# Performance work log

Measured on AMD Instinct MI355X. Metric: run time of the kernel, lower is better.

The kernel has to match this reference:

```python
import jax, jax.numpy as jnp
import numpy as np
from jax import lax

MARGIN = 0.2
NMAX = 1


def setup_inputs() -> dict:
    key = jax.random.key(0)
    k1, k2 = jax.random.split(key)
    N, D = 8192, 512
    imgs = jax.random.normal(k1, (N, D), dtype=jnp.float32)
    caps = jax.random.normal(k2, (N, D), dtype=jnp.float32)
    return {"imgs": imgs, "caps": caps}


def reference(imgs, caps):
    # scores[i, j] = <img_i, cap_j>  -> [N, N]
    scores = jnp.matmul(imgs, caps.T)
    diag = jnp.diagonal(scores)  # [N]
    s = scores - 2.0 * jnp.diag(diag)
    # top-nmax over columns (axis 0): hardest negative captions per caption slot
    max_c = lax.top_k(s.T, NMAX)[0].T  # [NMAX, N]
    # top-nmax over rows (axis 1): hardest negative images per image slot
    max_i = lax.top_k(s, NMAX)[0]      # [N, NMAX]
    neg_cap = jnp.sum(jnp.maximum(max_c + (MARGIN - diag)[None, :], 0.0))
    neg_img = jnp.sum(jnp.maximum(max_i + (MARGIN - diag)[:, None], 0.0))
    return neg_cap + neg_img
```

## Files before the change

### kernel.cpp

```cpp
#include <hip/hip_runtime.h>

#define N_ROWS 8192
#define DIM    512

typedef __attribute__((ext_vector_type(4))) float frag_cd;
typedef __attribute__((ext_vector_type(4))) int   v4i;
typedef __attribute__((ext_vector_type(8))) int   v8i;

__device__ __forceinline__ unsigned f2fp8(float x) {
    float a = fabsf(x);
    unsigned s = (__float_as_uint(x) >> 31) << 7;
    if (a < 0.015625f) return s;
    a = fminf(a, 448.f);
    unsigned u = __float_as_uint(a);
    u += 0x7FFFFu + ((u >> 20) & 1u);
    unsigned exp = (u >> 23) - 120u;
    unsigned mant = (u >> 20) & 7u;
    return s | (exp << 3) | mant;
}
__device__ __forceinline__ unsigned pack4fp8(float4 v) {
    return f2fp8(v.x) | (f2fp8(v.y) << 8) | (f2fp8(v.z) << 16) | (f2fp8(v.w) << 24);
}
__device__ __forceinline__ unsigned enc_f32(float f) {
    unsigned u = __float_as_uint(f);
    return (u & 0x80000000u) ? ~u : (u | 0x80000000u);
}
__device__ __forceinline__ float dec_f32(unsigned k) {
    return __uint_as_float((k & 0x80000000u) ? (k & 0x7FFFFFFFu) : ~k);
}


__global__ __launch_bounds__(256) void k_prep(const float* __restrict__ imgs,
                                              const float* __restrict__ caps,
                                              unsigned char* __restrict__ fimgs,
                                              unsigned char* __restrict__ fcaps,
                                              float* __restrict__ diag,
                                              unsigned* __restrict__ rowmax,
                                              unsigned* __restrict__ colmax,
                                              float* __restrict__ out) {
    const int b  = blockIdx.x;
    const int cr = b >> 2;
    const int t  = threadIdx.x;
    const int w = t >> 6, l = t & 63;
    const int row = ((b & 3) << 2) + w;
    if (b == 0 && t == 0) out[0] = 0.f;
    const int r = cr * 16 + row;
    const float* ar = imgs + (size_t)r * DIM + l * 8;
    const float* br = caps + (size_t)r * DIM + l * 8;
    float4 a0 = *(const float4*)ar, a1 = *(const float4*)(ar + 4);
    float4 b0 = *(const float4*)br, b1 = *(const float4*)(br + 4);
    uint2 oa, ob;
    oa.x = pack4fp8(a0); oa.y = pack4fp8(a1);
    ob.x = pack4fp8(b0); ob.y = pack4fp8(b1);
    const size_t addr = (size_t)cr * 8192 + (size_t)((l >> 4) << 11)
                      + (((l >> 1) & 1) << 10)
                      + ((((l >> 2) & 3) << 4) + row) * 16 + ((l & 1) << 3);
    *(uint2*)(fimgs + addr) = oa;
    *(uint2*)(fcaps + addr) = ob;
    float s = a0.x * b0.x + a0.y * b0.y + a0.z * b0.z + a0.w * b0.w
            + a1.x * b1.x + a1.y * b1.y + a1.z * b1.z + a1.w * b1.w;
    #pragma unroll
    for (int m = 1; m < 64; m <<= 1) s += __shfl_xor(s, m, 64);
    if (l == 0) { diag[r] = s; rowmax[r] = 0u; colmax[r] = 0u; }
}

__global__ __launch_bounds__(256, 2) void k_gemm(const unsigned char* __restrict__ A,
                                                 const unsigned char* __restrict__ B,
                                                 unsigned* __restrict__ rowmax,
                                                 unsigned* __restrict__ colmax) {
    const int tid = threadIdx.x;
    const int w = tid >> 6, lane = tid & 63;
    const int f = (int)blockIdx.x;
    const int jb = (f & 7) * 8 + ((f >> 3) & 7);
    const int ib = f >> 6;
    const int j0 = jb << 7, i0 = ib << 7;
    const int q = lane >> 4, l15 = lane & 15;
    const int wr = (w & 1) << 6, wc = (w >> 1) << 6;

    const unsigned char* Ab = A + (size_t)((i0 >> 4) + ((w & 1) << 2)) * 8192 + lane * 16;
    const unsigned char* Bb = B + (size_t)((j0 >> 4) + ((w >> 1) << 2)) * 8192 + lane * 16;

    frag_cd acc[4][4] = {};

    union U { v8i v; struct { v4i lo, hi; } s; };

    #pragma unroll
    for (int kp2 = 0; kp2 < 4; ++kp2) {
        U af[4], bf[4];
        #pragma unroll
        for (int r = 0; r < 4; ++r) {
            af[r].s.lo = *(const v4i*)(Ab + (size_t)r * 8192 + kp2 * 2048);
            af[r].s.hi = *(const v4i*)(Ab + (size_t)r * 8192 + kp2 * 2048 + 1024);
        }
        #pragma unroll
        for (int c = 0; c < 4; ++c) {
            bf[c].s.lo = *(const v4i*)(Bb + (size_t)c * 8192 + kp2 * 2048);
            bf[c].s.hi = *(const v4i*)(Bb + (size_t)c * 8192 + kp2 * 2048 + 1024);
        }
        #pragma unroll
        for (int r = 0; r < 4; ++r)
            #pragma unroll
            for (int c = 0; c < 4; ++c)
                acc[r][c] = __builtin_amdgcn_mfma_scale_f32_16x16x128_f8f6f4(
                    af[r].v, bf[c].v, acc[r][c], 0, 0,
                    0, 0x7F7F7F7F, 0, 0x7F7F7F7F);
    }

    const bool dblk = (i0 == j0);
    #pragma unroll
    for (int r = 0; r < 4; ++r)
        #pragma unroll
        for (int c = 0; c < 4; ++c)
            #pragma unroll
            for (int g = 0; g < 4; ++g) {
                float fv = acc[r][c][g];
                const int gi = wr + (r << 4) + (q << 2) + g;
                const int gj = wc + (c << 4) + l15;
                if (dblk && (i0 + gi) == (j0 + gj)) fv = -fv;
                acc[r][c][g] = fv;
            }

    #pragma unroll
    for (int r = 0; r < 4; ++r)
        #pragma unroll
        for (int g = 0; g < 4; ++g) {
            float m = fmaxf(fmaxf(acc[r][0][g], acc[r][1][g]),
                            fmaxf(acc[r][2][g], acc[r][3][g]));
            m = fmaxf(m, __shfl_xor(m, 1, 64));
            m = fmaxf(m, __shfl_xor(m, 2, 64));
            m = fmaxf(m, __shfl_xor(m, 4, 64));
            m = fmaxf(m, __shfl_xor(m, 8, 64));
            if (l15 == 0)
                atomicMax(&rowmax[i0 + wr + (r << 4) + (q << 2) + g], enc_f32(m));
        }
    #pragma unroll
    for (int c = 0; c < 4; ++c) {
        float m = acc[0][c][0];
        #pragma unroll
        for (int r = 0; r < 4; ++r)
            #pragma unroll
            for (int g = 0; g < 4; ++g) m = fmaxf(m, acc[r][c][g]);
        m = fmaxf(m, __shfl_xor(m, 16, 64));
        m = fmaxf(m, __shfl_xor(m, 32, 64));
        if (q == 0)
            atomicMax(&colmax[j0 + wc + (c << 4) + l15], enc_f32(m));
    }
}

__global__ __launch_bounds__(256) void k_final(const unsigned* __restrict__ rowmax,
                                               const unsigned* __restrict__ colmax,
                                               const float* __restrict__ diag,
                                               float* __restrict__ out) {
    const int idx = blockIdx.x * 256 + threadIdx.x;
    const float d = diag[idx];
    float s = fmaxf(dec_f32(rowmax[idx]) + 0.2f - d, 0.f)
            + fmaxf(dec_f32(colmax[idx]) + 0.2f - d, 0.f);
    #pragma unroll
    for (int m = 1; m < 64; m <<= 1) s += __shfl_xor(s, m, 64);
    __shared__ float red[4];
    if ((threadIdx.x & 63) == 0) red[threadIdx.x >> 6] = s;
    __syncthreads();
    if (threadIdx.x == 0)
        atomicAdd(out, red[0] + red[1] + red[2] + red[3]);
}

extern "C" void kernel_launch(void* const* d_in, const int* in_sizes, int n_in,
                              void* d_out, int out_size, void* d_ws, size_t ws_size,
                              hipStream_t stream) {
    const float* imgs = (const float*)d_in[0];
    const float* caps = (const float*)d_in[1];
    float* out = (float*)d_out;

    char* ws = (char*)d_ws;
    unsigned char* fimgs = (unsigned char*)ws;
    unsigned char* fcaps = (unsigned char*)(ws + 4194304);
    float*    diag   = (float*)   (ws + 8388608);
    unsigned* rowmax = (unsigned*)(ws + 8388608 + 32768);
    unsigned* colmax = (unsigned*)(ws + 8388608 + 65536);

    k_prep<<<2048, 256, 0, stream>>>(imgs, caps, fimgs, fcaps,
                                     diag, rowmax, colmax, out);
    k_gemm<<<4096, 256, 0, stream>>>(fimgs, fcaps, rowmax, colmax);
    k_final<<<N_ROWS / 256, 256, 0, stream>>>(rowmax, colmax, diag, out);
}
```

Before: 175.9 us.

## Double-buffer GEMM fragment loads and widen prep stores to 16-byte chunks

The GEMM kernel now prefetches the next K-slice's A/B fp8 fragments into a second register buffer while MFMAs run on the current slice. It also drops the launch-bounds occupancy hint of 2 blocks per CU. The prep kernel is restructured so each block handles 16 rows with one thread per 16-byte output chunk, issuing contiguous uint4 stores and reducing the diagonal through shared memory, with a quarter of the blocks. Costs are higher register pressure in the GEMM, which may lower occupancy, and strided float4 reads in prep.

```diff
diff --git a/kernel.cpp b/kernel.cpp
--- a/kernel.cpp
+++ b/kernel.cpp
@@ -38,36 +38,54 @@
                                               unsigned* __restrict__ rowmax,
                                               unsigned* __restrict__ colmax,
                                               float* __restrict__ out) {
-    const int b  = blockIdx.x;
-    const int cr = b >> 2;
+    const int cr = blockIdx.x;
     const int t  = threadIdx.x;
-    const int w = t >> 6, l = t & 63;
-    const int row = ((b & 3) << 2) + w;
-    if (b == 0 && t == 0) out[0] = 0.f;
-    const int r = cr * 16 + row;
-    const float* ar = imgs + (size_t)r * DIM + l * 8;
-    const float* br = caps + (size_t)r * DIM + l * 8;
-    float4 a0 = *(const float4*)ar, a1 = *(const float4*)(ar + 4);
-    float4 b0 = *(const float4*)br, b1 = *(const float4*)(br + 4);
-    uint2 oa, ob;
-    oa.x = pack4fp8(a0); oa.y = pack4fp8(a1);
-    ob.x = pack4fp8(b0); ob.y = pack4fp8(b1);
-    const size_t addr = (size_t)cr * 8192 + (size_t)((l >> 4) << 11)
-                      + (((l >> 1) & 1) << 10)
-                      + ((((l >> 2) & 3) << 4) + row) * 16 + ((l & 1) << 3);
-    *(uint2*)(fimgs + addr) = oa;
-    *(uint2*)(fcaps + addr) = ob;
-    float s = a0.x * b0.x + a0.y * b0.y + a0.z * b0.z + a0.w * b0.w
-            + a1.x * b1.x + a1.y * b1.y + a1.z * b1.z + a1.w * b1.w;
-    #pragma unroll
-    for (int m = 1; m < 64; m <<= 1) s += __shfl_xor(s, m, 64);
-    if (l == 0) { diag[r] = s; rowmax[r] = 0u; colmax[r] = 0u; }
-}
-
-__global__ __launch_bounds__(256, 2) void k_gemm(const unsigned char* __restrict__ A,
-                                                 const unsigned char* __restrict__ B,
-                                                 unsigned* __restrict__ rowmax,
-                                                 unsigned* __restrict__ colmax) {
+    if (cr == 0 && t == 0) out[0] = 0.f;
+    const int rin = t & 15;
+    const int q   = (t >> 4) & 3;
+    const int h   = (t >> 6) & 1;
+    const int kp2 = t >> 7;
+    const int row = cr * 16 + rin;
+    const int kc1 = kp2 * 128 + q * 32 + h * 16;
+    const int kc2 = kc1 + 256;
+    const float* ai = imgs + (size_t)row * DIM;
+    const float* bi = caps + (size_t)row * DIM;
+    float4 a[8], b[8];
+    #pragma unroll
+    for (int j = 0; j < 4; ++j) {
+        a[j]     = *(const float4*)(ai + kc1 + 4 * j);
+        a[4 + j] = *(const float4*)(ai + kc2 + 4 * j);
+        b[j]     = *(const float4*)(bi + kc1 + 4 * j);
+        b[4 + j] = *(const float4*)(bi + kc2 + 4 * j);
+    }
+    uint4 oa1 = make_uint4(pack4fp8(a[0]), pack4fp8(a[1]), pack4fp8(a[2]), pack4fp8(a[3]));
+    uint4 oa2 = make_uint4(pack4fp8(a[4]), pack4fp8(a[5]), pack4fp8(a[6]), pack4fp8(a[7]));
+    uint4 ob1 = make_uint4(pack4fp8(b[0]), pack4fp8(b[1]), pack4fp8(b[2]), pack4fp8(b[3]));
+    uint4 ob2 = make_uint4(pack4fp8(b[4]), pack4fp8(b[5]), pack4fp8(b[6]), pack4fp8(b[7]));
+    unsigned char* fA = fimgs + (size_t)cr * 8192 + t * 16;
+    unsigned char* fB = fcaps + (size_t)cr * 8192 + t * 16;
+    *(uint4*)fA = oa1; *(uint4*)(fA + 4096) = oa2;
+    *(uint4*)fB = ob1; *(uint4*)(fB + 4096) = ob2;
+    float s = 0.f;
+    #pragma unroll
+    for (int j = 0; j < 8; ++j)
+        s += a[j].x * b[j].x + a[j].y * b[j].y + a[j].z * b[j].z + a[j].w * b[j].w;
+    s += __shfl_xor(s, 16, 64);
+    s += __shfl_xor(s, 32, 64);
+    __shared__ float red[4][16];
+    if ((t & 63) < 16) red[t >> 6][rin] = s;
+    __syncthreads();
+    if (t < 16) {
+        diag[cr * 16 + t] = red[0][t] + red[1][t] + red[2][t] + red[3][t];
+        rowmax[cr * 16 + t] = 0u;
+        colmax[cr * 16 + t] = 0u;
+    }
+}
+
+__global__ __launch_bounds__(256) void k_gemm(const unsigned char* __restrict__ A,
+                                              const unsigned char* __restrict__ B,
+                                              unsigned* __restrict__ rowmax,
+                                              unsigned* __restrict__ colmax) {
     const int tid = threadIdx.x;
     const int w = tid >> 6, lane = tid & 63;
     const int f = (int)blockIdx.x;
@@ -83,26 +101,34 @@
     frag_cd acc[4][4] = {};
 
     union U { v8i v; struct { v4i lo, hi; } s; };
+    U af[2][4], bf[2][4];
+
+    #pragma unroll
+    for (int r = 0; r < 4; ++r) {
+        af[0][r].s.lo = *(const v4i*)(Ab + (size_t)r * 8192);
+        af[0][r].s.hi = *(const v4i*)(Ab + (size_t)r * 8192 + 1024);
+        bf[0][r].s.lo = *(const v4i*)(Bb + (size_t)r * 8192);
+        bf[0][r].s.hi = *(const v4i*)(Bb + (size_t)r * 8192 + 1024);
+    }
 
     #pragma unroll
     for (int kp2 = 0; kp2 < 4; ++kp2) {
-        U af[4], bf[4];
-        #pragma unroll
-        for (int r = 0; r < 4; ++r) {
-            af[r].s.lo = *(const v4i*)(Ab + (size_t)r * 8192 + kp2 * 2048);
-            af[r].s.hi = *(const v4i*)(Ab + (size_t)r * 8192 + kp2 * 2048 + 1024);
-        }
-        #pragma unroll
-        for (int c = 0; c < 4; ++c) {
-            bf[c].s.lo = *(const v4i*)(Bb + (size_t)c * 8192 + kp2 * 2048);
-            bf[c].s.hi = *(const v4i*)(Bb + (size_t)c * 8192 + kp2 * 2048 + 1024);
+        const int cur = kp2 & 1, nxt = cur ^ 1;
+        if (kp2 < 3) {
+            #pragma unroll
+            for (int r = 0; r < 4; ++r) {
+                af[nxt][r].s.lo = *(const v4i*)(Ab + (size_t)r * 8192 + (kp2 + 1) * 2048);
+                af[nxt][r].s.hi = *(const v4i*)(Ab + (size_t)r * 8192 + (kp2 + 1) * 2048 + 1024);
+                bf[nxt][r].s.lo = *(const v4i*)(Bb + (size_t)r * 8192 + (kp2 + 1) * 2048);
+                bf[nxt][r].s.hi = *(const v4i*)(Bb + (size_t)r * 8192 + (kp2 + 1) * 2048 + 1024);
+            }
         }
         #pragma unroll
         for (int r = 0; r < 4; ++r)
             #pragma unroll
             for (int c = 0; c < 4; ++c)
                 acc[r][c] = __builtin_amdgcn_mfma_scale_f32_16x16x128_f8f6f4(
-                    af[r].v, bf[c].v, acc[r][c], 0, 0,
+                    af[cur][r].v, bf[cur][c].v, acc[r][c], 0, 0,
                     0, 0x7F7F7F7F, 0, 0x7F7F7F7F);
     }
 
@@ -178,8 +204,8 @@
     unsigned* rowmax = (unsigned*)(ws + 8388608 + 32768);
     unsigned* colmax = (unsigned*)(ws + 8388608 + 65536);
 
-    k_prep<<<2048, 256, 0, stream>>>(imgs, caps, fimgs, fcaps,
-                                     diag, rowmax, colmax, out);
+    k_prep<<<512, 256, 0, stream>>>(imgs, caps, fimgs, fcaps,
+                                    diag, rowmax, colmax, out);
     k_gemm<<<4096, 256, 0, stream>>>(fimgs, fcaps, rowmax, colmax);
     k_final<<<N_ROWS / 256, 256, 0, stream>>>(rowmax, colmax, diag, out);
 }
```

Result: slower. 188.9 us (+7.4%).
